# Kernel optimization log

Measured on AMD Instinct MI355X. Metric: run time of the kernel, lower is better.

Reference implementation:

```python
import jax, jax.numpy as jnp
import numpy as np

N_NODES = 100_000
N_EDGES = 1_600_000  # random edges; self-loops appended (add_self_edges_networkx)
IN_FEATS = 64
N_HIDDEN = 64
N_CLASSES = 40


def setup_inputs() -> dict:
    key = jax.random.key(0)
    ks = jax.random.split(key, 10)
    features = jax.random.normal(ks[0], (N_NODES, IN_FEATS), jnp.float32)
    self_loops = jnp.arange(N_NODES, dtype=jnp.int32)
    src = jnp.concatenate([jax.random.randint(ks[1], (N_EDGES,), 0, N_NODES, jnp.int32), self_loops])
    dst = jnp.concatenate([jax.random.randint(ks[2], (N_EDGES,), 0, N_NODES, jnp.int32), self_loops])
    labels = jax.random.randint(ks[3], (N_NODES,), 0, N_CLASSES, jnp.int32)
    mask = jnp.ones((N_NODES,), bool)
    s = 0.05
    W0 = jax.random.normal(ks[4], (IN_FEATS, N_HIDDEN), jnp.float32) * s
    b0 = jnp.zeros((N_HIDDEN,), jnp.float32)
    W1 = jax.random.normal(ks[5], (N_HIDDEN, N_HIDDEN), jnp.float32) * s
    b1 = jnp.zeros((N_HIDDEN,), jnp.float32)
    W2 = jax.random.normal(ks[6], (N_HIDDEN, N_CLASSES), jnp.float32) * s
    b2 = jnp.zeros((N_CLASSES,), jnp.float32)
    return {"features": features, "W0": W0, "b0": b0, "W1": W1, "b1": b1,
            "W2": W2, "b2": b2, "src": src, "dst": dst,
            "labels": labels, "mask": mask}


def reference(features, W0, b0, W1, b1, W2, b2, src, dst, labels, mask):
    # gcn_msg: pass src 'h'; gcn_reduce: sum over incoming messages;
    # NodeApplyModule: linear (+ activation on non-final layers).
    def gcn_layer(h, W, b, act):
        agg = jax.ops.segment_sum(h[src], dst, num_segments=N_NODES)  # gather -> sum reduce
        h = agg @ W + b
        return jax.nn.relu(h) if act else h

    h = gcn_layer(features, W0, b0, act=True)
    h = gcn_layer(h, W1, b1, act=True)
    rep = gcn_layer(h, W2, b2, act=False)  # [N, n_classes]

    # loss: fn_reduce=log_softmax over dim=0 (as written in the source), nll sum / count
    logp = jax.nn.log_softmax(rep, axis=0)
    picked = jnp.take_along_axis(logp, labels[:, None].astype(jnp.int32), axis=1)[:, 0]
    maskf = mask.astype(jnp.float32)
    loss = -jnp.sum(picked * maskf) / jnp.sum(maskf)
    return rep, loss
```

## Files before the change

### kernel.cpp

```cpp
#include <hip/hip_runtime.h>
#include <hip/hip_bf16.h>
#include <hip/hip_fp16.h>

#define NCLS 40

typedef __attribute__((ext_vector_type(8))) _Float16 half8;

#define EPB 16384
#define MAXB1 128
#define MAXNB 104

__global__ void bucket_hist(const int* __restrict__ dst, int E, int nb,
                            int* __restrict__ blockHist) {
    __shared__ int cnt[MAXNB];
    int t = threadIdx.x;
    for (int i = t; i < nb; i += 256) cnt[i] = 0;
    __syncthreads();
    int base = blockIdx.x * EPB;
    int end = min(base + EPB, E);
    for (int i = base + t; i < end; i += 256) atomicAdd(&cnt[dst[i] >> 10], 1);
    __syncthreads();
    for (int i = t; i < nb; i += 256) blockHist[blockIdx.x * nb + i] = cnt[i];
}

__global__ void bucket_scan(const int* __restrict__ blockHist, int nB1, int nb,
                            int* __restrict__ blockBase, int* __restrict__ bucketOffs,
                            int* __restrict__ offs, int N, int E) {
    __shared__ int h[MAXB1 * MAXNB];
    __shared__ int btot[MAXNB];
    __shared__ int boffs[MAXNB + 1];
    int t = threadIdx.x;
    int total = nB1 * nb;
    for (int i = t; i < total; i += 128) h[i] = blockHist[i];
    __syncthreads();
    for (int b = t; b < nb; b += 128) {
        int run = 0;
        for (int i = 0; i < nB1; ++i) { int v = h[i * nb + b]; h[i * nb + b] = run; run += v; }
        btot[b] = run;
    }
    __syncthreads();
    if (t == 0) {
        int run = 0;
        for (int b = 0; b < nb; ++b) { boffs[b] = run; run += btot[b]; }
        boffs[nb] = run;
    }
    __syncthreads();
    for (int b = t; b < nb; b += 128) {
        int bo = boffs[b];
        for (int i = 0; i < nB1; ++i) h[i * nb + b] += bo;
    }
    __syncthreads();
    for (int i = t; i < total; i += 128) blockBase[i] = h[i];
    for (int b = t; b <= nb; b += 128) bucketOffs[b] = boffs[b];
    if (t == 0) offs[N] = E;
}

__global__ void bucket_place(const int* __restrict__ src, const int* __restrict__ dst, int E,
                             int nb, const int* __restrict__ blockBase,
                             unsigned* __restrict__ tmp) {
    __shared__ int cur[MAXNB];
    int t = threadIdx.x;
    for (int i = t; i < nb; i += 256) cur[i] = blockBase[blockIdx.x * nb + i];
    __syncthreads();
    int base = blockIdx.x * EPB;
    int end = min(base + EPB, E);
    for (int i = base + t; i < end; i += 256) {
        int d = dst[i];
        int s = src[i];
        unsigned pack = ((unsigned)(d & 1023) << 17) | (unsigned)s;
        int pos = atomicAdd(&cur[d >> 10], 1);
        tmp[pos] = pack;
    }
}

__global__ __launch_bounds__(512) void bucket_finalize(const unsigned* __restrict__ tmp,
                                                       const int* __restrict__ bucketOffs,
                                                       int N, int* __restrict__ offs,
                                                       int* __restrict__ esrc) {
    __shared__ int cnt[1024];
    __shared__ int wsum[8];
    int b = blockIdx.x;
    int t = threadIdx.x;
    int bstart = bucketOffs[b], bend = bucketOffs[b + 1];
    cnt[t] = 0;
    cnt[t + 512] = 0;
    __syncthreads();
    for (int i = bstart + t; i < bend; i += 512) atomicAdd(&cnt[tmp[i] >> 17], 1);
    __syncthreads();
    int c0 = cnt[2 * t], c1 = cnt[2 * t + 1];
    int s = c0 + c1;
    int lane = t & 63, w = t >> 6;
    int ssc = s;
    for (int off = 1; off < 64; off <<= 1) {
        int v = __shfl_up(ssc, off, 64);
        if (lane >= off) ssc += v;
    }
    if (lane == 63) wsum[w] = ssc;
    __syncthreads();
    int wo = 0;
#pragma unroll
    for (int k = 0; k < 8; ++k)
        if (k < w) wo += wsum[k];
    int excl = (ssc - s) + wo + bstart;
    __syncthreads();
    int node0 = (b << 10) + 2 * t;
    if (node0 < N) offs[node0] = excl;
    if (node0 + 1 < N) offs[node0 + 1] = excl + c0;
    cnt[2 * t] = excl;
    cnt[2 * t + 1] = excl + c0;
    __syncthreads();
    for (int i = bstart + t; i < bend; i += 512) {
        unsigned p = tmp[i];
        int pos = atomicAdd(&cnt[p >> 17], 1);
        esrc[pos] = (int)(p & 0x1FFFFu);
    }
}

__global__ __launch_bounds__(256, 4) void gemm_v3(const float* __restrict__ X,
                                                  const float* __restrict__ W,
                                                  const float* __restrict__ bias,
                                                  void* __restrict__ out, int N, int FO,
                                                  int outHalf) {
    int lane = threadIdx.x & 63;
    int waveId = (blockIdx.x * blockDim.x + threadIdx.x) >> 6;
    int nWaves = (gridDim.x * blockDim.x) >> 6;
    int cl = lane < FO ? lane : 0;

    float w[64];
#pragma unroll
    for (int k = 0; k < 64; ++k) w[k] = W[k * FO + cl];
    float bv = 0.f;
    if (bias != nullptr && lane < FO) bv = bias[lane];

    float* outF = (float*)out;
    _Float16* outH = (_Float16*)out;

    int row = waveId;
    float xv = (row < N) ? X[(size_t)row * 64 + lane] : 0.f;
    for (; row < N; row += nWaves) {
        int nrow = row + nWaves;
        float nxt = (nrow < N) ? X[(size_t)nrow * 64 + lane] : 0.f;
        float acc = bv;
#pragma unroll
        for (int k = 0; k < 64; ++k) {
            float xk = __uint_as_float(__builtin_amdgcn_readlane(__float_as_uint(xv), k));
            acc = fmaf(xk, w[k], acc);
        }
        if (lane < FO) {
            if (outHalf) outH[(size_t)row * FO + lane] = (_Float16)acc;
            else         outF[(size_t)row * FO + lane] = acc;
        }
        xv = nxt;
    }
}

__global__ void agg64h_kernel(const _Float16* __restrict__ t, const int* __restrict__ offs,
                              const int* __restrict__ esrc, const float* __restrict__ bias,
                              void* __restrict__ out, int N, int doRelu, int outHalf) {
    int gid = blockIdx.x * blockDim.x + threadIdx.x;
    int node = gid >> 6;
    if (node >= N) return;
    int lane = threadIdx.x & 63;
    int sub = lane >> 3;
    int c8 = lane & 7;
    int beg = offs[node], end = offs[node + 1];
    float a[8];
#pragma unroll
    for (int k = 0; k < 8; ++k) a[k] = 0.f;
    int j = beg + sub;
    for (; j + 8 < end; j += 16) {
        int s0 = esrc[j];
        int s1 = esrc[j + 8];
        half8 v0 = *(const half8*)(t + (size_t)s0 * 64 + c8 * 8);
        half8 v1 = *(const half8*)(t + (size_t)s1 * 64 + c8 * 8);
#pragma unroll
        for (int k = 0; k < 8; ++k) a[k] += (float)v0[k] + (float)v1[k];
    }
    if (j < end) {
        int s0 = esrc[j];
        half8 v0 = *(const half8*)(t + (size_t)s0 * 64 + c8 * 8);
#pragma unroll
        for (int k = 0; k < 8; ++k) a[k] += (float)v0[k];
    }
#pragma unroll
    for (int k = 0; k < 8; ++k) {
        a[k] += __shfl_down(a[k], 32, 64);
        a[k] += __shfl_down(a[k], 16, 64);
        a[k] += __shfl_down(a[k], 8, 64);
    }
    if (sub == 0) {
        if (bias != nullptr) {
#pragma unroll
            for (int k = 0; k < 8; ++k) a[k] += bias[c8 * 8 + k];
        }
        if (doRelu) {
#pragma unroll
            for (int k = 0; k < 8; ++k) a[k] = fmaxf(a[k], 0.f);
        }
        if (outHalf) {
            half8 hv;
#pragma unroll
            for (int k = 0; k < 8; ++k) hv[k] = (_Float16)a[k];
            *(half8*)((_Float16*)out + (size_t)node * 64 + c8 * 8) = hv;
        } else {
            float* po = (float*)out + (size_t)node * 64 + c8 * 8;
            float4 r0 = {a[0], a[1], a[2], a[3]};
            float4 r1 = {a[4], a[5], a[6], a[7]};
            *(float4*)(po) = r0;
            *(float4*)(po + 4) = r1;
        }
    }
}

__global__ void loss_pass(const float* __restrict__ rep, const int* __restrict__ labels, int N,
                          double* __restrict__ colSum, double* __restrict__ pickedSum,
                          int* __restrict__ cnt) {
    const int G = 8;
    const int ROWS = 512;
    int t = threadIdx.x;
    int c = t % NCLS;
    int g = t / NCLS;
    int base = blockIdx.x * ROWS;
    int lim = min(base + ROWS, N);
    double sumLoc = 0.0, pickLoc = 0.0;
    int cntLoc = 0;
    for (int r = base + g; r < lim; r += G) {
        float v = rep[(size_t)r * NCLS + c];
        sumLoc += exp((double)v);
        if (labels[r] == c) { pickLoc += (double)v; cntLoc++; }
    }
    __shared__ double colP[G][NCLS];
    __shared__ int cntP[G][NCLS];
    __shared__ double waveP[5];
    colP[g][c] = sumLoc;
    cntP[g][c] = cntLoc;
    __syncthreads();
    if (g == 0) {
        double tot = 0.0;
        int ctot = 0;
        for (int gg = 0; gg < G; ++gg) { tot += colP[gg][c]; ctot += cntP[gg][c]; }
        atomicAdd(&colSum[c], tot);
        if (ctot) atomicAdd(&cnt[c], ctot);
    }
    double wv = pickLoc;
    for (int off = 32; off; off >>= 1) wv += __shfl_down(wv, off, 64);
    if ((t & 63) == 0) waveP[t >> 6] = wv;
    __syncthreads();
    if (t == 0) {
        double s = 0.0;
        for (int i = 0; i < 5; ++i) s += waveP[i];
        atomicAdd(pickedSum, s);
    }
}

__global__ void finalize_kernel(const double* __restrict__ colSum, const int* __restrict__ cnt,
                                const double* __restrict__ pickedSum, int N,
                                float* __restrict__ lossOut) {
    int t = threadIdx.x;
    double term = 0.0;
    if (t < NCLS) term = (double)cnt[t] * log(colSum[t]);
    for (int off = 32; off; off >>= 1) term += __shfl_down(term, off, 64);
    if (t == 0) lossOut[0] = (float)((term - pickedSum[0]) / (double)N);
}

extern "C" void kernel_launch(void* const* d_in, const int* in_sizes, int n_in,
                              void* d_out, int out_size, void* d_ws, size_t ws_size,
                              hipStream_t stream) {
    const float* features = (const float*)d_in[0];
    const float* W0 = (const float*)d_in[1];
    const float* b0 = (const float*)d_in[2];
    const float* W1 = (const float*)d_in[3];
    const float* b1 = (const float*)d_in[4];
    const float* W2 = (const float*)d_in[5];
    const float* b2 = (const float*)d_in[6];
    const int* src = (const int*)d_in[7];
    const int* dst = (const int*)d_in[8];
    const int* labels = (const int*)d_in[9];

    const int N = in_sizes[0] / 64;
    const int E = in_sizes[7];
    const int NC = in_sizes[6];

    char* ws = (char*)d_ws;
    size_t off = 0;
    auto alloc = [&](size_t bytes) -> void* {
        void* p = ws + off;
        off = (off + bytes + 255) & ~(size_t)255;
        return p;
    };
    int* offs      = (int*)alloc((size_t)(N + 1) * 4);
    int* esrc      = (int*)alloc((size_t)E * 4);
    _Float16* t0   = (_Float16*)alloc((size_t)N * 64 * 2);
    float* h1      = (float*)alloc((size_t)N * 64 * 4);
    _Float16* h2   = (_Float16*)alloc((size_t)N * 64 * 2);
    int* blockHist = (int*)alloc((size_t)MAXB1 * MAXNB * 4);
    int* blockBase = (int*)alloc((size_t)MAXB1 * MAXNB * 4);
    int* bucketOffs= (int*)alloc((size_t)(MAXNB + 1) * 4);
    char* red      = (char*)alloc(512);
    double* colSum    = (double*)red;
    double* pickedSum = (double*)(red + 320);
    int* cntRed       = (int*)(red + 328);

    unsigned* tmp = (unsigned*)t0;
    float* t2 = h1;

    float* rep = (float*)d_out;
    float* lossOut = rep + (size_t)N * NC;

    const int nb  = (N + 1023) >> 10;
    const int nB1 = (E + EPB - 1) / EPB;

    hipMemsetAsync(red, 0, 512, stream);

    bucket_hist<<<nB1, 256, 0, stream>>>(dst, E, nb, blockHist);
    bucket_scan<<<1, 128, 0, stream>>>(blockHist, nB1, nb, blockBase, bucketOffs, offs, N, E);
    bucket_place<<<nB1, 256, 0, stream>>>(src, dst, E, nb, blockBase, tmp);
    bucket_finalize<<<nb, 512, 0, stream>>>(tmp, bucketOffs, N, offs, esrc);

    const int nodeWaveBlocks = (N * 64 + 255) / 256;

    gemm_v3<<<2048, 256, 0, stream>>>(features, W0, nullptr, t0, N, 64, 1);
    agg64h_kernel<<<nodeWaveBlocks, 256, 0, stream>>>(t0, offs, esrc, b0, h1, N, 1, 0);
    gemm_v3<<<2048, 256, 0, stream>>>(h1, W1, nullptr, t0, N, 64, 1);
    agg64h_kernel<<<nodeWaveBlocks, 256, 0, stream>>>(t0, offs, esrc, b1, h2, N, 1, 1);
    agg64h_kernel<<<nodeWaveBlocks, 256, 0, stream>>>(h2, offs, esrc, nullptr, t2, N, 0, 0);
    gemm_v3<<<2048, 256, 0, stream>>>(t2, W2, b2, rep, N, NC, 0);

    loss_pass<<<(N + 511) / 512, 320, 0, stream>>>(rep, labels, N, colSum, pickedSum, cntRed);
    finalize_kernel<<<1, 64, 0, stream>>>(colSum, cntRed, pickedSum, N, lossOut);
}
```

Before: 426.9 us.

## Use fp16 dot2 GEMM, fp16 aggregation accumulators and fp16 intermediates throughout

The GEMM now stores weights as packed half2 and uses v_dot2 fp16 instructions with two accumulators, and it can read fp16 inputs directly. The aggregation kernel accumulates in packed half8 vectors instead of fp32 and always writes fp16 outputs, so the fp32 intermediate buffers (h1, t2) shrink to fp16 and memory traffic falls. The histogram kernel spreads its shared-memory atomics over four copies to reduce contention, and the memset is folded into bucket_scan. Accumulating in fp16 over about 17 edges per node, plus an fp16 cast of the input features, reduces accuracy and may overflow or lose tolerance.

Measured after the change: 433.9 us. Within noise of the previous version (+1.6%).

```diff
diff --git a/kernel.cpp b/kernel.cpp
--- a/kernel.cpp
+++ b/kernel.cpp
@@ -5,6 +5,8 @@
 #define NCLS 40
 
 typedef __attribute__((ext_vector_type(8))) _Float16 half8;
+typedef __attribute__((ext_vector_type(2))) _Float16 half2h;
+union H2U { half2h h; unsigned u; };
 
 #define EPB 16384
 #define MAXB1 128
@@ -12,24 +14,27 @@
 
 __global__ void bucket_hist(const int* __restrict__ dst, int E, int nb,
                             int* __restrict__ blockHist) {
-    __shared__ int cnt[MAXNB];
-    int t = threadIdx.x;
-    for (int i = t; i < nb; i += 256) cnt[i] = 0;
-    __syncthreads();
+    __shared__ int cnt[4][MAXNB];
+    int t = threadIdx.x;
+    for (int i = t; i < 4 * MAXNB; i += 256) cnt[i / MAXNB][i % MAXNB] = 0;
+    __syncthreads();
+    int bk = t & 3;
     int base = blockIdx.x * EPB;
     int end = min(base + EPB, E);
-    for (int i = base + t; i < end; i += 256) atomicAdd(&cnt[dst[i] >> 10], 1);
-    __syncthreads();
-    for (int i = t; i < nb; i += 256) blockHist[blockIdx.x * nb + i] = cnt[i];
+    for (int i = base + t; i < end; i += 256) atomicAdd(&cnt[bk][dst[i] >> 10], 1);
+    __syncthreads();
+    for (int i = t; i < nb; i += 256)
+        blockHist[blockIdx.x * nb + i] = cnt[0][i] + cnt[1][i] + cnt[2][i] + cnt[3][i];
 }
 
 __global__ void bucket_scan(const int* __restrict__ blockHist, int nB1, int nb,
                             int* __restrict__ blockBase, int* __restrict__ bucketOffs,
-                            int* __restrict__ offs, int N, int E) {
+                            int* __restrict__ offs, int N, int E, int* __restrict__ red32) {
     __shared__ int h[MAXB1 * MAXNB];
     __shared__ int btot[MAXNB];
     __shared__ int boffs[MAXNB + 1];
     int t = threadIdx.x;
+    if (t < 128) red32[t] = 0;
     int total = nB1 * nb;
     for (int i = t; i < total; i += 128) h[i] = blockHist[i];
     __syncthreads();
@@ -116,47 +121,66 @@
     }
 }
 
-__global__ __launch_bounds__(256, 4) void gemm_v3(const float* __restrict__ X,
-                                                  const float* __restrict__ W,
-                                                  const float* __restrict__ bias,
-                                                  void* __restrict__ out, int N, int FO,
-                                                  int outHalf) {
+__global__ __launch_bounds__(256) void gemm_fdot(const void* __restrict__ X, int xHalf,
+                                                 const float* __restrict__ W,
+                                                 const float* __restrict__ bias,
+                                                 void* __restrict__ out, int outHalf,
+                                                 int N, int FO) {
     int lane = threadIdx.x & 63;
     int waveId = (blockIdx.x * blockDim.x + threadIdx.x) >> 6;
     int nWaves = (gridDim.x * blockDim.x) >> 6;
     int cl = lane < FO ? lane : 0;
-
-    float w[64];
-#pragma unroll
-    for (int k = 0; k < 64; ++k) w[k] = W[k * FO + cl];
-    float bv = 0.f;
-    if (bias != nullptr && lane < FO) bv = bias[lane];
-
+    int p = lane & 31;
+
+    H2U wh[32];
+#pragma unroll
+    for (int j = 0; j < 32; ++j)
+        wh[j].h = half2h{(_Float16)W[(2 * j) * FO + cl], (_Float16)W[(2 * j + 1) * FO + cl]};
+    float gb = 0.f;
+    if (bias != nullptr && lane < FO) gb = bias[lane];
+
+    const unsigned* Xh = (const unsigned*)X;
+    const float2* Xf = (const float2*)X;
     float* outF = (float*)out;
     _Float16* outH = (_Float16*)out;
 
+    auto loadX = [&](int row) -> H2U {
+        H2U r; r.u = 0;
+        if (row < N) {
+            if (xHalf) r.u = Xh[(size_t)row * 32 + p];
+            else {
+                float2 f = Xf[(size_t)row * 32 + p];
+                r.h = half2h{(_Float16)f.x, (_Float16)f.y};
+            }
+        }
+        return r;
+    };
+
     int row = waveId;
-    float xv = (row < N) ? X[(size_t)row * 64 + lane] : 0.f;
+    H2U xp = loadX(row);
     for (; row < N; row += nWaves) {
-        int nrow = row + nWaves;
-        float nxt = (nrow < N) ? X[(size_t)nrow * 64 + lane] : 0.f;
-        float acc = bv;
-#pragma unroll
-        for (int k = 0; k < 64; ++k) {
-            float xk = __uint_as_float(__builtin_amdgcn_readlane(__float_as_uint(xv), k));
-            acc = fmaf(xk, w[k], acc);
+        H2U nxt = loadX(row + nWaves);
+        float y0 = gb, y1 = 0.f;
+#pragma unroll
+        for (int j2 = 0; j2 < 32; j2 += 2) {
+            H2U r0, r1;
+            r0.u = __builtin_amdgcn_readlane(xp.u, j2);
+            r1.u = __builtin_amdgcn_readlane(xp.u, j2 + 1);
+            y0 = __builtin_amdgcn_fdot2(r0.h, wh[j2].h, y0, false);
+            y1 = __builtin_amdgcn_fdot2(r1.h, wh[j2 + 1].h, y1, false);
         }
+        float y = y0 + y1;
         if (lane < FO) {
-            if (outHalf) outH[(size_t)row * FO + lane] = (_Float16)acc;
-            else         outF[(size_t)row * FO + lane] = acc;
+            if (outHalf) outH[(size_t)row * FO + lane] = (_Float16)y;
+            else         outF[(size_t)row * FO + lane] = y;
         }
-        xv = nxt;
+        xp = nxt;
     }
 }
 
 __global__ void agg64h_kernel(const _Float16* __restrict__ t, const int* __restrict__ offs,
                               const int* __restrict__ esrc, const float* __restrict__ bias,
-                              void* __restrict__ out, int N, int doRelu, int outHalf) {
+                              _Float16* __restrict__ out, int N, int doRelu) {
     int gid = blockIdx.x * blockDim.x + threadIdx.x;
     int node = gid >> 6;
     if (node >= N) return;
@@ -164,24 +188,25 @@
     int sub = lane >> 3;
     int c8 = lane & 7;
     int beg = offs[node], end = offs[node + 1];
-    float a[8];
-#pragma unroll
-    for (int k = 0; k < 8; ++k) a[k] = 0.f;
+    half8 acc0 = {};
+    half8 acc1 = {};
     int j = beg + sub;
     for (; j + 8 < end; j += 16) {
         int s0 = esrc[j];
         int s1 = esrc[j + 8];
         half8 v0 = *(const half8*)(t + (size_t)s0 * 64 + c8 * 8);
         half8 v1 = *(const half8*)(t + (size_t)s1 * 64 + c8 * 8);
-#pragma unroll
-        for (int k = 0; k < 8; ++k) a[k] += (float)v0[k] + (float)v1[k];
+        acc0 += v0;
+        acc1 += v1;
     }
     if (j < end) {
         int s0 = esrc[j];
-        half8 v0 = *(const half8*)(t + (size_t)s0 * 64 + c8 * 8);
-#pragma unroll
-        for (int k = 0; k < 8; ++k) a[k] += (float)v0[k];
-    }
+        acc0 += *(const half8*)(t + (size_t)s0 * 64 + c8 * 8);
+    }
+    half8 acc = acc0 + acc1;
+    float a[8];
+#pragma unroll
+    for (int k = 0; k < 8; ++k) a[k] = (float)acc[k];
 #pragma unroll
     for (int k = 0; k < 8; ++k) {
         a[k] += __shfl_down(a[k], 32, 64);
@@ -189,26 +214,15 @@
         a[k] += __shfl_down(a[k], 8, 64);
     }
     if (sub == 0) {
-        if (bias != nullptr) {
-#pragma unroll
-            for (int k = 0; k < 8; ++k) a[k] += bias[c8 * 8 + k];
+        half8 hv;
+#pragma unroll
+        for (int k = 0; k < 8; ++k) {
+            float v = a[k];
+            if (bias != nullptr) v += bias[c8 * 8 + k];
+            if (doRelu) v = fmaxf(v, 0.f);
+            hv[k] = (_Float16)v;
         }
-        if (doRelu) {
-#pragma unroll
-            for (int k = 0; k < 8; ++k) a[k] = fmaxf(a[k], 0.f);
-        }
-        if (outHalf) {
-            half8 hv;
-#pragma unroll
-            for (int k = 0; k < 8; ++k) hv[k] = (_Float16)a[k];
-            *(half8*)((_Float16*)out + (size_t)node * 64 + c8 * 8) = hv;
-        } else {
-            float* po = (float*)out + (size_t)node * 64 + c8 * 8;
-            float4 r0 = {a[0], a[1], a[2], a[3]};
-            float4 r1 = {a[4], a[5], a[6], a[7]};
-            *(float4*)(po) = r0;
-            *(float4*)(po + 4) = r1;
-        }
+        *(half8*)(out + (size_t)node * 64 + c8 * 8) = hv;
     }
 }
 
@@ -290,9 +304,8 @@
     };
     int* offs      = (int*)alloc((size_t)(N + 1) * 4);
     int* esrc      = (int*)alloc((size_t)E * 4);
-    _Float16* t0   = (_Float16*)alloc((size_t)N * 64 * 2);
-    float* h1      = (float*)alloc((size_t)N * 64 * 4);
-    _Float16* h2   = (_Float16*)alloc((size_t)N * 64 * 2);
+    _Float16* bufA = (_Float16*)alloc((size_t)N * 64 * 2);
+    _Float16* bufB = (_Float16*)alloc((size_t)N * 64 * 2);
     int* blockHist = (int*)alloc((size_t)MAXB1 * MAXNB * 4);
     int* blockBase = (int*)alloc((size_t)MAXB1 * MAXNB * 4);
     int* bucketOffs= (int*)alloc((size_t)(MAXNB + 1) * 4);
@@ -301,8 +314,7 @@
     double* pickedSum = (double*)(red + 320);
     int* cntRed       = (int*)(red + 328);
 
-    unsigned* tmp = (unsigned*)t0;
-    float* t2 = h1;
+    unsigned* tmp = (unsigned*)bufA;
 
     float* rep = (float*)d_out;
     float* lossOut = rep + (size_t)N * NC;
@@ -310,21 +322,20 @@
     const int nb  = (N + 1023) >> 10;
     const int nB1 = (E + EPB - 1) / EPB;
 
-    hipMemsetAsync(red, 0, 512, stream);
-
     bucket_hist<<<nB1, 256, 0, stream>>>(dst, E, nb, blockHist);
-    bucket_scan<<<1, 128, 0, stream>>>(blockHist, nB1, nb, blockBase, bucketOffs, offs, N, E);
+    bucket_scan<<<1, 128, 0, stream>>>(blockHist, nB1, nb, blockBase, bucketOffs, offs, N, E,
+                                       (int*)red);
     bucket_place<<<nB1, 256, 0, stream>>>(src, dst, E, nb, blockBase, tmp);
     bucket_finalize<<<nb, 512, 0, stream>>>(tmp, bucketOffs, N, offs, esrc);
 
     const int nodeWaveBlocks = (N * 64 + 255) / 256;
 
-    gemm_v3<<<2048, 256, 0, stream>>>(features, W0, nullptr, t0, N, 64, 1);
-    agg64h_kernel<<<nodeWaveBlocks, 256, 0, stream>>>(t0, offs, esrc, b0, h1, N, 1, 0);
-    gemm_v3<<<2048, 256, 0, stream>>>(h1, W1, nullptr, t0, N, 64, 1);
-    agg64h_kernel<<<nodeWaveBlocks, 256, 0, stream>>>(t0, offs, esrc, b1, h2, N, 1, 1);
-    agg64h_kernel<<<nodeWaveBlocks, 256, 0, stream>>>(h2, offs, esrc, nullptr, t2, N, 0, 0);
-    gemm_v3<<<2048, 256, 0, stream>>>(t2, W2, b2, rep, N, NC, 0);
+    gemm_fdot<<<2048, 256, 0, stream>>>(features, 0, W0, nullptr, bufA, 1, N, 64);
+    agg64h_kernel<<<nodeWaveBlocks, 256, 0, stream>>>(bufA, offs, esrc, b0, bufB, N, 1);
+    gemm_fdot<<<2048, 256, 0, stream>>>(bufB, 1, W1, nullptr, bufA, 1, N, 64);
+    agg64h_kernel<<<nodeWaveBlocks, 256, 0, stream>>>(bufA, offs, esrc, b1, bufB, N, 1);
+    agg64h_kernel<<<nodeWaveBlocks, 256, 0, stream>>>(bufB, offs, esrc, nullptr, bufA, N, 0);
+    gemm_fdot<<<2048, 256, 0, stream>>>(bufA, 1, W2, b2, rep, 0, N, NC);
 
     loss_pass<<<(N + 511) / 512, 320, 0, stream>>>(rep, labels, N, colSum, pickedSum, cntRed);
     finalize_kernel<<<1, 64, 0, stream>>>(colSum, cntRed, pickedSum, N, lossOut);
```
